# Kernel optimization log

Measured on AMD Instinct MI355X. Metric: run time of the kernel, lower is better.

Reference implementation:

```python
import jax, jax.numpy as jnp
import numpy as np

NX, NY, NC, NT = 320, 320, 20, 25


def ifft2c(x):
    # centered orthonormal 2D inverse FFT over axes (0,1)
    return jnp.fft.fftshift(
        jnp.fft.ifft2(jnp.fft.ifftshift(x, axes=(0, 1)), axes=(0, 1), norm='ortho'),
        axes=(0, 1))


def warp_bilinear(im, flw):
    # im: [Nx,Ny] complex, flw: [Nx,Ny,2] float pixel displacements
    # Sparse motion matrix application = bilinear gather at (x+u, y+v)
    Nx, Ny = im.shape
    gx, gy = jnp.meshgrid(jnp.arange(Nx, dtype=jnp.float32),
                          jnp.arange(Ny, dtype=jnp.float32), indexing='ij')
    xs = jnp.clip(gx + flw[..., 0], 0.0, Nx - 1.0)
    ys = jnp.clip(gy + flw[..., 1], 0.0, Ny - 1.0)
    x0 = jnp.floor(xs).astype(jnp.int32)
    y0 = jnp.floor(ys).astype(jnp.int32)
    x1 = jnp.minimum(x0 + 1, Nx - 1)
    y1 = jnp.minimum(y0 + 1, Ny - 1)
    wx = xs - x0.astype(jnp.float32)
    wy = ys - y0.astype(jnp.float32)
    return (im[x0, y0] * ((1 - wx) * (1 - wy))
            + im[x1, y0] * (wx * (1 - wy))
            + im[x0, y1] * ((1 - wx) * wy)
            + im[x1, y1] * (wx * wy))


def setup_inputs() -> dict:
    key = jax.random.key(0)
    ks = jax.random.split(key, 6)
    return {
        'kspace_re': jax.random.normal(ks[0], (NX, NY, NC), dtype=jnp.float32),
        'kspace_im': jax.random.normal(ks[1], (NX, NY, NC), dtype=jnp.float32),
        'mask': jax.random.uniform(ks[2], (NX, NY, NC, NT), dtype=jnp.float32),
        'smaps_re': jax.random.normal(ks[3], (NX, NY, NC), dtype=jnp.float32),
        'smaps_im': jax.random.normal(ks[4], (NX, NY, NC), dtype=jnp.float32),
        'flow': jax.random.normal(ks[5], (NX, NY, 2, NT), dtype=jnp.float32),
    }


def reference(kspace_re, kspace_im, mask, smaps_re, smaps_im, flow):
    kspace = kspace_re + 1j * kspace_im          # [Nx,Ny,Nc]
    smaps = smaps_re + 1j * smaps_im             # [Nx,Ny,Nc]
    # masked kspace for all motion states: [Nx,Ny,Nc,Nt]
    ksp_t = kspace[..., None] * mask.astype(kspace.dtype)
    coil_ims = ifft2c(ksp_t)                     # [Nx,Ny,Nc,Nt]
    # coil combine: sum_c ifft2c(k*m) * conj(smaps) -> [Nx,Ny,Nt]
    im_t = jnp.sum(coil_ims * jnp.conj(smaps)[..., None], axis=2)
    # per-frame sparse motion warp, then sum over motion states
    warped = jax.vmap(warp_bilinear, in_axes=(2, 3))(im_t, flow)  # [Nt,Nx,Ny]
    out = jnp.sum(warped, axis=0)                # [Nx,Ny] complex
    return jnp.stack([out.real, out.imag])       # [2,Nx,Ny] float32 view
```

## Files before the change

### kernel.cpp

```cpp
#include <hip/hip_runtime.h>
#include <hip/hip_fp16.h>
#include <math.h>

#define NXY 320
#define NC 20
#define NT 25
#define NPIX 102400
#define PI_F 3.14159265358979f
#define TWOPI_F 6.28318530717959f

__device__ __forceinline__ float2 cmul(float2 a, float2 b) {
    return make_float2(a.x * b.x - a.y * b.y, a.x * b.y + a.y * b.x);
}

struct Tw {
    float2 st[6];
    float  sgn[6];
    float2 w5[5];
    int J;
};

__device__ __forceinline__ void tw_init(Tw& t) {
    const int lane = threadIdx.x & 63;
    #pragma unroll
    for (int s = 0; s < 6; ++s) {
        const int h = 32 >> s;
        const bool up = (lane & h) != 0;
        t.sgn[s] = up ? -1.0f : 1.0f;
        if (up) {
            float ss, cc;
            __sincosf(PI_F * (float)(lane & (h - 1)) / (float)h, &ss, &cc);
            t.st[s] = make_float2(cc, ss);
        } else {
            t.st[s] = make_float2(1.0f, 0.0f);
        }
    }
    t.J = (int)(__brev((unsigned)lane) >> 26);
    t.w5[0] = make_float2(1.0f, 0.0f);
    #pragma unroll
    for (int r = 1; r < 5; ++r) {
        float ss, cc;
        __sincosf(TWOPI_F * (float)(r * t.J) / 320.0f, &ss, &cc);
        t.w5[r] = make_float2(cc, ss);
    }
}

template <int K>
__device__ __forceinline__ void fft320xK(const Tw& t, float2 (&x)[K][5], float2 (&out)[K][5]) {
    #pragma unroll
    for (int s = 0; s < 6; ++s) {
        const int h = 32 >> s;
        #pragma unroll
        for (int r = 0; r < 5; ++r) {
            #pragma unroll
            for (int k = 0; k < K; ++k) {
                float ox = __shfl_xor(x[k][r].x, h);
                float oy = __shfl_xor(x[k][r].y, h);
                float dx = fmaf(t.sgn[s], x[k][r].x, ox);
                float dy = fmaf(t.sgn[s], x[k][r].y, oy);
                x[k][r].x = dx * t.st[s].x - dy * t.st[s].y;
                x[k][r].y = dx * t.st[s].y + dy * t.st[s].x;
            }
        }
    }
    const float W5x[5] = {1.0f, 0.309016994f, -0.809016994f, -0.809016994f, 0.309016994f};
    const float W5y[5] = {0.0f, 0.951056516f, 0.587785252f, -0.587785252f, -0.951056516f};
    #pragma unroll
    for (int k = 0; k < K; ++k) {
        float2 T[5];
        T[0] = x[k][0];
        #pragma unroll
        for (int r = 1; r < 5; ++r) T[r] = cmul(x[k][r], t.w5[r]);
        #pragma unroll
        for (int s5 = 0; s5 < 5; ++s5) {
            float2 acc = T[0];
            #pragma unroll
            for (int r = 1; r < 5; ++r) {
                const int kk = (r * s5) % 5;
                acc.x += T[r].x * W5x[kk] - T[r].y * W5y[kk];
                acc.y += T[r].x * W5y[kk] + T[r].y * W5x[kk];
            }
            out[k][s5] = acc;
        }
    }
}

__global__ __launch_bounds__(256) void k_prep_smaps(const float* __restrict__ smr,
                                                    const float* __restrict__ smi,
                                                    float2* __restrict__ smapsC) {
    const int p0 = blockIdx.x * 64;
    __shared__ float s_r[64 * 21];
    __shared__ float s_i[64 * 21];
    for (int j = threadIdx.x; j < 64 * NC; j += blockDim.x) {
        int p = j / NC, c = j - p * NC;
        s_r[p * 21 + c] = smr[(size_t)p0 * NC + j];
        s_i[p * 21 + c] = smi[(size_t)p0 * NC + j];
    }
    __syncthreads();
    for (int j = threadIdx.x; j < 64 * NC; j += blockDim.x) {
        int c = j >> 6, p = j & 63;
        int pg = p0 + p;
        int m = pg / NXY, n = pg - m * NXY;
        float sgn = (((m + n) & 1) ? -1.0f : 1.0f) * (1.0f / 320.0f);
        smapsC[(size_t)c * NPIX + pg] = make_float2(s_r[p * 21 + c] * sgn,
                                                    -s_i[p * 21 + c] * sgn);
    }
}

__global__ __launch_bounds__(256) void k_perm_smaps(const float2* __restrict__ smapsC,
                                                    __half2* __restrict__ smapsP) {
    const int c = blockIdx.x;
    const int s5 = blockIdx.y;
    const int v0 = blockIdx.z * 64;
    __shared__ __half2 t2[64 * 65];
    for (int j = threadIdx.x; j < 64 * 64; j += blockDim.x) {
        int ur = j >> 6, vc = j & 63;
        float2 v = smapsC[(size_t)c * NPIX + (size_t)(s5 * 64 + ur) * NXY + v0 + vc];
        t2[ur * 65 + vc] = __floats2half2_rn(v.x, v.y);
    }
    __syncthreads();
    for (int j = threadIdx.x; j < 64 * 64; j += blockDim.x) {
        int vr = j >> 6, lane = j & 63;
        int J = (int)(__brev((unsigned)lane) >> 26);
        smapsP[(size_t)((c * NXY + v0 + vr) * 5 + s5) * 64 + lane] = t2[J * 65 + vr];
    }
}

__global__ __launch_bounds__(256) void k_prep_input(const float* __restrict__ ksr,
                                                    const float* __restrict__ ksi,
                                                    const float* __restrict__ mask,
                                                    __half2* __restrict__ X0,
                                                    int t0, int G) {
    const int p0 = blockIdx.x * 16;
    __shared__ float s_mask[16 * 501];
    __shared__ float s_kr[16 * 21];
    __shared__ float s_ki[16 * 21];
    for (int j = threadIdx.x; j < 16 * NC; j += blockDim.x) {
        int p = j / NC, c = j - p * NC;
        s_kr[p * 21 + c] = ksr[(size_t)p0 * NC + j];
        s_ki[p * 21 + c] = ksi[(size_t)p0 * NC + j];
    }
    for (int j = threadIdx.x; j < 16 * 500; j += blockDim.x) {
        int p = j / 500, col = j - p * 500;
        s_mask[p * 501 + col] = mask[(size_t)p0 * 500 + j];
    }
    __syncthreads();
    const int p = threadIdx.x & 15;
    const int g16 = threadIdx.x >> 4;
    const int pg = p0 + p;
    const int m = pg / NXY;
    const int n = pg - m * NXY;
    const float sgn = ((m + n) & 1) ? -1.0f : 1.0f;
    #pragma unroll
    for (int c = 0; c < NC; ++c) {
        const float kr = s_kr[p * 21 + c] * sgn;
        const float ki = s_ki[p * 21 + c] * sgn;
        for (int tc = g16; tc < G; tc += 16) {
            const int q = c * G + tc;
            const float mk = s_mask[p * 501 + c * NT + t0 + tc];
            X0[(size_t)q * NPIX + pg] = __floats2half2_rn(kr * mk, ki * mk);
        }
    }
}

__global__ __launch_bounds__(256) void k_fft_rows(const __half2* __restrict__ X0,
                                                  __half2* __restrict__ Z, int G) {
    const int mtile = blockIdx.x;
    const int tc = blockIdx.y;
    const int c = blockIdx.z;
    const int q = c * G + tc;
    const int wave = threadIdx.x >> 6;
    const int lane = threadIdx.x & 63;
    const int m0 = mtile * 16;
    __shared__ __half2 tile[NXY * 17];
    Tw t;
    tw_init(t);
    const __half2* src = X0 + (size_t)q * NPIX;
    float2 x[4][5], out[4][5];
    #pragma unroll
    for (int k = 0; k < 4; ++k) {
        const __half2* row = src + (size_t)(m0 + wave + 4 * k) * NXY + lane * 5;
        #pragma unroll
        for (int r = 0; r < 5; ++r) x[k][r] = __half22float2(row[r]);
    }
    fft320xK<4>(t, x, out);
    #pragma unroll
    for (int k = 0; k < 4; ++k) {
        const int mm = wave + 4 * k;
        #pragma unroll
        for (int s5 = 0; s5 < 5; ++s5) {
            int v = t.J + 64 * s5;
            tile[v * 17 + mm] = __floats2half2_rn(out[k][s5].x, out[k][s5].y);
        }
    }
    __syncthreads();
    __half2* dst = Z + (size_t)q * NPIX + m0;
    for (int j = threadIdx.x; j < NXY * 16; j += blockDim.x) {
        int mm = j & 15, v = j >> 4;
        dst[(size_t)v * NXY + mm] = tile[v * 17 + mm];
    }
}

__global__ __launch_bounds__(256) void k_fft_cols_combine(const __half2* __restrict__ Z,
                                                          const __half2* __restrict__ smapsP,
                                                          __half2* __restrict__ imtP,
                                                          int t0, int G) {
    const int vtile = blockIdx.x;
    const int tc = blockIdx.y;
    const int half = blockIdx.z;
    const int wave = threadIdx.x >> 6;
    const int lane = threadIdx.x & 63;
    const int v0 = vtile * 8;
    const int vA = v0 + wave;
    const int vB = v0 + 4 + wave;
    __shared__ __half2 tile[NXY * 9];
    Tw t;
    tw_init(t);
    float2 acc[2][5];
    #pragma unroll
    for (int k = 0; k < 2; ++k)
        #pragma unroll
        for (int s5 = 0; s5 < 5; ++s5) acc[k][s5] = make_float2(0.f, 0.f);
    const int c0 = half * 10;
    for (int c = c0; c < c0 + 10; ++c) {
        const __half2* zc = Z + (size_t)(c * G + tc) * NPIX;
        float2 x[2][5], out[2][5];
        const __half2* colA = zc + (size_t)vA * NXY + lane * 5;
        const __half2* colB = zc + (size_t)vB * NXY + lane * 5;
        #pragma unroll
        for (int r = 0; r < 5; ++r) {
            x[0][r] = __half22float2(colA[r]);
            x[1][r] = __half22float2(colB[r]);
        }
        fft320xK<2>(t, x, out);
        const __half2* spA = smapsP + (size_t)((c * NXY + vA) * 5) * 64 + lane;
        const __half2* spB = smapsP + (size_t)((c * NXY + vB) * 5) * 64 + lane;
        #pragma unroll
        for (int s5 = 0; s5 < 5; ++s5) {
            float2 smA = __half22float2(spA[s5 * 64]);
            float2 smB = __half22float2(spB[s5 * 64]);
            float2 ta = cmul(out[0][s5], smA);
            float2 tb = cmul(out[1][s5], smB);
            acc[0][s5].x += ta.x; acc[0][s5].y += ta.y;
            acc[1][s5].x += tb.x; acc[1][s5].y += tb.y;
        }
    }
    #pragma unroll
    for (int s5 = 0; s5 < 5; ++s5) {
        int u = t.J + 64 * s5;
        tile[u * 9 + wave] = __floats2half2_rn(acc[0][s5].x, acc[0][s5].y);
        tile[u * 9 + 4 + wave] = __floats2half2_rn(acc[1][s5].x, acc[1][s5].y);
    }
    __syncthreads();
    __half2* dst = imtP + (size_t)(half * NT + t0 + tc) * NPIX + v0;
    for (int j = threadIdx.x; j < NXY * 8; j += blockDim.x) {
        int vv = j & 7, u = j >> 3;
        dst[(size_t)u * NXY + vv] = tile[u * 9 + vv];
    }
}

__global__ __launch_bounds__(256) void k_warp_sum(const __half2* __restrict__ imtP,
                                                  const float* __restrict__ flow,
                                                  float* __restrict__ out) {
    const int p0 = blockIdx.x * 256;
    const int tid = threadIdx.x;
    __shared__ float s_fl[2 * NT * 257];
    for (int j = tid; j < 256 * 50; j += 256) {
        int pp = j / 50, rem = j - pp * 50;
        int d = rem / 25, tt = rem - d * 25;
        s_fl[(d * NT + tt) * 257 + pp] = flow[(size_t)p0 * 50 + j];
    }
    __syncthreads();
    const int p = p0 + tid;
    const int x = p / NXY, y = p - x * NXY;
    const float fx = (float)x, fy = (float)y;
    float ar = 0.f, ai = 0.f;
    for (int t = 0; t < NT; ++t) {
        float u = s_fl[t * 257 + tid];
        float v = s_fl[(NT + t) * 257 + tid];
        float xs = fminf(fmaxf(fx + u, 0.0f), 319.0f);
        float ys = fminf(fmaxf(fy + v, 0.0f), 319.0f);
        float x0f = floorf(xs), y0f = floorf(ys);
        int x0 = (int)x0f, y0 = (int)y0f;
        int x1 = min(x0 + 1, NXY - 1), y1 = min(y0 + 1, NXY - 1);
        float wx = xs - x0f, wy = ys - y0f;
        const __half2* b0 = imtP + (size_t)t * NPIX;
        const __half2* b1 = imtP + (size_t)(NT + t) * NPIX;
        int i00 = x0 * NXY + y0, i01 = x0 * NXY + y1;
        int i10 = x1 * NXY + y0, i11 = x1 * NXY + y1;
        float2 c00 = __half22float2(b0[i00]); float2 d00 = __half22float2(b1[i00]);
        float2 c01 = __half22float2(b0[i01]); float2 d01 = __half22float2(b1[i01]);
        float2 c10 = __half22float2(b0[i10]); float2 d10 = __half22float2(b1[i10]);
        float2 c11 = __half22float2(b0[i11]); float2 d11 = __half22float2(b1[i11]);
        c00.x += d00.x; c00.y += d00.y;
        c01.x += d01.x; c01.y += d01.y;
        c10.x += d10.x; c10.y += d10.y;
        c11.x += d11.x; c11.y += d11.y;
        float w00 = (1.f - wx) * (1.f - wy), w01 = (1.f - wx) * wy;
        float w10 = wx * (1.f - wy), w11 = wx * wy;
        ar += c00.x * w00 + c01.x * w01 + c10.x * w10 + c11.x * w11;
        ai += c00.y * w00 + c01.y * w01 + c10.y * w10 + c11.y * w11;
    }
    out[p] = ar;
    out[NPIX + p] = ai;
}

extern "C" void kernel_launch(void* const* d_in, const int* in_sizes, int n_in,
                              void* d_out, int out_size, void* d_ws, size_t ws_size,
                              hipStream_t stream) {
    const float* ksr = (const float*)d_in[0];
    const float* ksi = (const float*)d_in[1];
    const float* mask = (const float*)d_in[2];
    const float* smr = (const float*)d_in[3];
    const float* smi = (const float*)d_in[4];
    const float* flow = (const float*)d_in[5];
    float* out = (float*)d_out;

    char* ws = (char*)d_ws;
    const size_t smapsC_bytes = (size_t)NC * NPIX * sizeof(float2);
    const size_t smapsP_bytes = (size_t)NC * NPIX * sizeof(__half2);
    const size_t imtP_bytes = (size_t)2 * NT * NPIX * sizeof(__half2);
    const size_t fixed = smapsC_bytes + smapsP_bytes + imtP_bytes;
    const size_t per_t = (size_t)2 * NC * NPIX * sizeof(__half2);

    int G = 1;
    if (ws_size > fixed + per_t) {
        size_t g = (ws_size - fixed) / per_t;
        G = (int)(g > (size_t)NT ? (size_t)NT : g);
    }
    if (G < 1) G = 1;

    float2* smapsC = (float2*)ws;
    __half2* smapsP = (__half2*)(ws + smapsC_bytes);
    __half2* imtP = (__half2*)(ws + smapsC_bytes + smapsP_bytes);
    __half2* X0 = (__half2*)(ws + fixed);
    __half2* Z = (__half2*)(ws + fixed + (size_t)NC * G * NPIX * sizeof(__half2));

    k_prep_smaps<<<NPIX / 64, 256, 0, stream>>>(smr, smi, smapsC);
    k_perm_smaps<<<dim3(NC, 5, 5), 256, 0, stream>>>(smapsC, smapsP);
    for (int t0 = 0; t0 < NT; t0 += G) {
        int g = (NT - t0) < G ? (NT - t0) : G;
        k_prep_input<<<NPIX / 16, 256, 0, stream>>>(ksr, ksi, mask, X0, t0, g);
        k_fft_rows<<<dim3(20, g, NC), 256, 0, stream>>>(X0, Z, g);
        k_fft_cols_combine<<<dim3(40, g, 2), 256, 0, stream>>>(Z, smapsP, imtP, t0, g);
    }
    k_warp_sum<<<NPIX / 256, 256, 0, stream>>>(imtP, flow, out);
}
```

Baseline: 823.6 us.

## Fuse mask multiply into row FFT and drop the masked-kspace intermediate

Sign-modulated, half-precision k-space is now precomputed once per coil into a small buffer. The mask multiply moves into the row-FFT load, so the large per-frame masked k-space array (X0) is never written or read back. The row-FFT grid is reordered so all coil/frame blocks for the same row tile run together, letting neighbouring blocks share mask cache lines in L2. The price is a strided, uncoalesced mask gather inside the FFT kernel. Freeing X0 also lets more frames fit per workspace batch.

Measured after the change: 889.1 us. 1.08x slower.

```diff
diff --git a/kernel.cpp b/kernel.cpp
--- a/kernel.cpp
+++ b/kernel.cpp
@@ -126,62 +126,57 @@
     }
 }
 
-__global__ __launch_bounds__(256) void k_prep_input(const float* __restrict__ ksr,
-                                                    const float* __restrict__ ksi,
-                                                    const float* __restrict__ mask,
-                                                    __half2* __restrict__ X0,
-                                                    int t0, int G) {
-    const int p0 = blockIdx.x * 16;
-    __shared__ float s_mask[16 * 501];
-    __shared__ float s_kr[16 * 21];
-    __shared__ float s_ki[16 * 21];
-    for (int j = threadIdx.x; j < 16 * NC; j += blockDim.x) {
+__global__ __launch_bounds__(256) void k_prep_ks(const float* __restrict__ ksr,
+                                                 const float* __restrict__ ksi,
+                                                 __half2* __restrict__ ksS) {
+    const int p0 = blockIdx.x * 64;
+    __shared__ float s_r[64 * 21];
+    __shared__ float s_i[64 * 21];
+    for (int j = threadIdx.x; j < 64 * NC; j += blockDim.x) {
         int p = j / NC, c = j - p * NC;
-        s_kr[p * 21 + c] = ksr[(size_t)p0 * NC + j];
-        s_ki[p * 21 + c] = ksi[(size_t)p0 * NC + j];
-    }
-    for (int j = threadIdx.x; j < 16 * 500; j += blockDim.x) {
-        int p = j / 500, col = j - p * 500;
-        s_mask[p * 501 + col] = mask[(size_t)p0 * 500 + j];
-    }
-    __syncthreads();
-    const int p = threadIdx.x & 15;
-    const int g16 = threadIdx.x >> 4;
-    const int pg = p0 + p;
-    const int m = pg / NXY;
-    const int n = pg - m * NXY;
-    const float sgn = ((m + n) & 1) ? -1.0f : 1.0f;
-    #pragma unroll
-    for (int c = 0; c < NC; ++c) {
-        const float kr = s_kr[p * 21 + c] * sgn;
-        const float ki = s_ki[p * 21 + c] * sgn;
-        for (int tc = g16; tc < G; tc += 16) {
-            const int q = c * G + tc;
-            const float mk = s_mask[p * 501 + c * NT + t0 + tc];
-            X0[(size_t)q * NPIX + pg] = __floats2half2_rn(kr * mk, ki * mk);
-        }
-    }
-}
-
-__global__ __launch_bounds__(256) void k_fft_rows(const __half2* __restrict__ X0,
-                                                  __half2* __restrict__ Z, int G) {
-    const int mtile = blockIdx.x;
-    const int tc = blockIdx.y;
-    const int c = blockIdx.z;
-    const int q = c * G + tc;
+        s_r[p * 21 + c] = ksr[(size_t)p0 * NC + j];
+        s_i[p * 21 + c] = ksi[(size_t)p0 * NC + j];
+    }
+    __syncthreads();
+    for (int j = threadIdx.x; j < 64 * NC; j += blockDim.x) {
+        int c = j >> 6, p = j & 63;
+        int pg = p0 + p;
+        int m = pg / NXY, n = pg - m * NXY;
+        float sgn = ((m + n) & 1) ? -1.0f : 1.0f;
+        ksS[(size_t)c * NPIX + pg] =
+            __floats2half2_rn(s_r[p * 21 + c] * sgn, s_i[p * 21 + c] * sgn);
+    }
+}
+
+__global__ __launch_bounds__(256) void k_fft_rows(const float* __restrict__ mask,
+                                                  const __half2* __restrict__ ksS,
+                                                  __half2* __restrict__ Z,
+                                                  int t0, int G) {
+    const int q = blockIdx.x;
+    const int mtile = blockIdx.y;
+    const int c = q / G;
+    const int tc = q - c * G;
+    const int cq = c * NT + t0 + tc;
     const int wave = threadIdx.x >> 6;
     const int lane = threadIdx.x & 63;
     const int m0 = mtile * 16;
     __shared__ __half2 tile[NXY * 17];
     Tw t;
     tw_init(t);
-    const __half2* src = X0 + (size_t)q * NPIX;
+    const __half2* ks_c = ksS + (size_t)c * NPIX;
+    const float* mk_c = mask + (size_t)cq;
     float2 x[4][5], out[4][5];
     #pragma unroll
     for (int k = 0; k < 4; ++k) {
-        const __half2* row = src + (size_t)(m0 + wave + 4 * k) * NXY + lane * 5;
-        #pragma unroll
-        for (int r = 0; r < 5; ++r) x[k][r] = __half22float2(row[r]);
+        const int pbase = (m0 + wave + 4 * k) * NXY + lane * 5;
+        const __half2* kp = ks_c + pbase;
+        const float* mp = mk_c + (size_t)pbase * (NC * NT);
+        #pragma unroll
+        for (int r = 0; r < 5; ++r) {
+            float2 kv = __half22float2(kp[r]);
+            float mkv = mp[(size_t)r * (NC * NT)];
+            x[k][r] = make_float2(kv.x * mkv, kv.y * mkv);
+        }
     }
     fft320xK<4>(t, x, out);
     #pragma unroll
@@ -319,9 +314,10 @@
     char* ws = (char*)d_ws;
     const size_t smapsC_bytes = (size_t)NC * NPIX * sizeof(float2);
     const size_t smapsP_bytes = (size_t)NC * NPIX * sizeof(__half2);
+    const size_t ksS_bytes = (size_t)NC * NPIX * sizeof(__half2);
     const size_t imtP_bytes = (size_t)2 * NT * NPIX * sizeof(__half2);
-    const size_t fixed = smapsC_bytes + smapsP_bytes + imtP_bytes;
-    const size_t per_t = (size_t)2 * NC * NPIX * sizeof(__half2);
+    const size_t fixed = smapsC_bytes + smapsP_bytes + ksS_bytes + imtP_bytes;
+    const size_t per_t = (size_t)NC * NPIX * sizeof(__half2);
 
     int G = 1;
     if (ws_size > fixed + per_t) {
@@ -332,16 +328,16 @@
 
     float2* smapsC = (float2*)ws;
     __half2* smapsP = (__half2*)(ws + smapsC_bytes);
-    __half2* imtP = (__half2*)(ws + smapsC_bytes + smapsP_bytes);
-    __half2* X0 = (__half2*)(ws + fixed);
-    __half2* Z = (__half2*)(ws + fixed + (size_t)NC * G * NPIX * sizeof(__half2));
+    __half2* ksS = (__half2*)(ws + smapsC_bytes + smapsP_bytes);
+    __half2* imtP = (__half2*)(ws + smapsC_bytes + smapsP_bytes + ksS_bytes);
+    __half2* Z = (__half2*)(ws + fixed);
 
     k_prep_smaps<<<NPIX / 64, 256, 0, stream>>>(smr, smi, smapsC);
     k_perm_smaps<<<dim3(NC, 5, 5), 256, 0, stream>>>(smapsC, smapsP);
+    k_prep_ks<<<NPIX / 64, 256, 0, stream>>>(ksr, ksi, ksS);
     for (int t0 = 0; t0 < NT; t0 += G) {
         int g = (NT - t0) < G ? (NT - t0) : G;
-        k_prep_input<<<NPIX / 16, 256, 0, stream>>>(ksr, ksi, mask, X0, t0, g);
-        k_fft_rows<<<dim3(20, g, NC), 256, 0, stream>>>(X0, Z, g);
+        k_fft_rows<<<dim3(NC * g, 20), 256, 0, stream>>>(mask, ksS, Z, t0, g);
         k_fft_cols_combine<<<dim3(40, g, 2), 256, 0, stream>>>(Z, smapsP, imtP, t0, g);
     }
     k_warp_sum<<<NPIX / 256, 256, 0, stream>>>(imtP, flow, out);
```
